# Kernel optimization log

Hardware: AMD Instinct MI355X
Metric: run time of the kernel (lower is better)

## Reference

```python
import jax, jax.numpy as jnp
import numpy as np

B, T, N, F = 4, 12, 4096, 32
NG = 14  # 14 gate GNNs: fx,fh,ix,ih,cx,ch,ox,oh,i,im,g,gm,o,om


def setup_inputs() -> dict:
    key = jax.random.key(0)
    k1, k2, k3 = jax.random.split(key, 3)
    x = jax.random.normal(k1, (B, T, N, F), dtype=jnp.float32)
    # weighted adjacency, scaled like row-normalized so adj@x stays O(1)
    adj = jax.random.uniform(k2, (B, N, N), dtype=jnp.float32) / N
    W = jax.random.normal(k3, (NG, F, 2 * F), dtype=jnp.float32) * (1.0 / np.sqrt(F))
    b = jnp.zeros((NG, 2 * F), dtype=jnp.float32)
    return {"x": x, "adj": adj, "W": W, "b": b}


def _wgc(v, adj, Wi, bi):
    # WeightedGraphConv: adj-matmul -> Dense(2F) -> GLU
    y = jnp.matmul(adj, v)                 # [B,N,F]
    z = jnp.matmul(y, Wi) + bi             # [B,N,2F]
    ls, rs = jnp.split(z, 2, axis=-1)
    return ls * jax.nn.sigmoid(rs)         # [B,N,F]


def reference(x, adj, W, b):
    Bb, Tt, Nn, Ff = x.shape
    ones = jnp.ones((Bb, Nn, Ff), dtype=x.dtype)
    h0, c0, m0 = ones, ones, ones

    def step(carry, xt):
        h, c, m = carry
        g = lambda i, v: _wgc(v, adj, W[i], b[i])
        f = jax.nn.sigmoid(g(0, xt) + g(1, h))     # forget
        i = jax.nn.sigmoid(g(2, xt) + g(3, h))     # input
        o = jax.nn.sigmoid(g(6, xt) + g(7, h))     # output
        c_new = f * c + i * jnp.tanh(g(4, xt) + g(5, h))
        h_mid = o * jnp.tanh(c_new)
        # memory-state gates (has_memory_state=True)
        i2 = jax.nn.sigmoid(g(8, h_mid) + g(9, m))
        gg = jax.nn.sigmoid(g(10, h_mid) + g(11, m))
        o2 = jax.nn.sigmoid(g(12, h_mid) + g(13, m))
        m_new = i2 * m + (1.0 - i2) * gg
        h_new = m_new * o2
        return (h_new, c_new, m_new), h_new

    (last_h, last_c, last_m), hs = jax.lax.scan(step, (h0, c0, m0), jnp.swapaxes(x, 0, 1))
    hidden_states = jnp.swapaxes(hs, 0, 1)  # [B,T,N,F]
    return hidden_states, last_h, last_c, last_m
```

## Files before the change

### kernel.cpp

```cpp
#include <hip/hip_runtime.h>


typedef __bf16 bf16_t;
typedef __bf16 bf16x8 __attribute__((ext_vector_type(8)));
typedef float  f32x4  __attribute__((ext_vector_type(4)));

#define DI __device__ __forceinline__

#define BB 4
#define TT 12
#define NN 4096
#define FF 32

DI float sigm(float x)  { return __builtin_amdgcn_rcpf(1.f + __expf(-x)); }
DI float tanh_f(float x){ float e = __expf(2.f * x); return 1.f - 2.f * __builtin_amdgcn_rcpf(e + 1.f); }

__global__ __launch_bounds__(256) void conv_adj_k(const float* __restrict__ a,
                                                  bf16_t* __restrict__ o) {
    size_t i = ((size_t)blockIdx.x * 256 + threadIdx.x) * 8;
    float4 v0 = *(const float4*)(a + i);
    float4 v1 = *(const float4*)(a + i + 4);
    union { uint4 u; bf16_t h[8]; } t;
    t.h[0] = (bf16_t)v0.x; t.h[1] = (bf16_t)v0.y; t.h[2] = (bf16_t)v0.z; t.h[3] = (bf16_t)v0.w;
    t.h[4] = (bf16_t)v1.x; t.h[5] = (bf16_t)v1.y; t.h[6] = (bf16_t)v1.z; t.h[7] = (bf16_t)v1.w;
    *(uint4*)(o + i) = t.u;
}

__global__ __launch_bounds__(256) void xpose_k(const float* __restrict__ x,
                                               bf16_t* __restrict__ xT) {
    const int b = blockIdx.z, t = blockIdx.y, n0 = blockIdx.x * 64;
    const int tid = threadIdx.x;
    __shared__ float tile[64][33];
    const float* src = x + (((size_t)(b * TT + t)) * NN + n0) * FF;
#pragma unroll
    for (int rr = 0; rr < 2; ++rr) {
        int idx = rr * 256 + tid;
        int row = idx >> 3, seg = idx & 7;
        float4 v = *(const float4*)(src + row * FF + seg * 4);
        tile[row][seg * 4 + 0] = v.x; tile[row][seg * 4 + 1] = v.y;
        tile[row][seg * 4 + 2] = v.z; tile[row][seg * 4 + 3] = v.w;
    }
    __syncthreads();
    const int f = tid >> 3, seg = tid & 7;
    union { uint4 u; bf16_t h[8]; } o;
#pragma unroll
    for (int j = 0; j < 8; ++j) o.h[j] = (bf16_t)tile[seg * 8 + j][f];
    *(uint4*)&xT[((size_t)(b * 384 + t * FF + f)) * NN + n0 + seg * 8] = o.u;
}

__global__ __launch_bounds__(256) void make_wfrag_k(const float* __restrict__ W,
                                                    bf16_t* __restrict__ Wf) {
    const int g = blockIdx.x, tid = threadIdx.x;
    const int ct = tid >> 6, lane = tid & 63;
    const int k0 = (lane >> 4) * 8, col = ct * 16 + (lane & 15);
    union { uint4 u; bf16_t h[8]; } t;
#pragma unroll
    for (int j = 0; j < 8; ++j) t.h[j] = (bf16_t)W[(g * 32 + k0 + j) * 64 + col];
    *(uint4*)&Wf[((g * 4 + ct) * 64 + lane) * 8] = t.u;
}

__global__ __launch_bounds__(256) void init_k(bf16_t* h_bf, bf16_t* hm_bf,
                                              float* c, float* m,
                                              float* Y1, float* Y2) {
    const int idx = blockIdx.x * 256 + threadIdx.x;
    Y1[idx] = 0.f;
    Y2[idx] = 0.f;
    if (idx < 524288) {
        const int b = idx >> 17, r = idx & 131071;
        h_bf[idx] = (bf16_t)1.f;
        hm_bf[(size_t)b * 262144 + 131072 + r] = (bf16_t)1.f;
        c[idx] = 1.f;
        m[idx] = 1.f;
    }
}

template <bool ABF, int S, int BS0, int BS1>
__global__ __launch_bounds__(256, 4) void gemm_splitk(const void* __restrict__ Ap,
                                                      const bf16_t* __restrict__ p0,
                                                      const bf16_t* __restrict__ p1,
                                                      float* __restrict__ Y) {
    const int b = blockIdx.z;
    const int row0 = blockIdx.x * 64;
    const int slice = blockIdx.y;
    const int tid = threadIdx.x, wave = tid >> 6, lane = tid & 63;
    const int mrow = lane & 15, quad = lane >> 4;
    __shared__ __align__(16) bf16_t Vs[64 * 256];
    const f32x4 zero = {0.f, 0.f, 0.f, 0.f};
    f32x4 acc[4];
#pragma unroll
    for (int i = 0; i < 4; ++i) acc[i] = zero;
    const int row = row0 + wave * 16 + mrow;
    const size_t arow = ((size_t)b << 24) + (size_t)row * NN;

    for (int stg = 0; stg < 4; ++stg) {
        const int k0 = slice * 1024 + stg * 256;
        bf16x8 af[8];
        if constexpr (ABF) {
            const bf16_t* ab = (const bf16_t*)Ap + arow + k0 + quad * 8;
#pragma unroll
            for (int s = 0; s < 8; ++s) af[s] = *(const bf16x8*)(ab + s * 32);
        } else {
            const float* ab = (const float*)Ap + arow + k0 + quad * 8;
#pragma unroll
            for (int s = 0; s < 8; ++s) {
                float4 v0 = *(const float4*)(ab + s * 32);
                float4 v1 = *(const float4*)(ab + s * 32 + 4);
                af[s][0] = (bf16_t)v0.x; af[s][1] = (bf16_t)v0.y;
                af[s][2] = (bf16_t)v0.z; af[s][3] = (bf16_t)v0.w;
                af[s][4] = (bf16_t)v1.x; af[s][5] = (bf16_t)v1.y;
                af[s][6] = (bf16_t)v1.z; af[s][7] = (bf16_t)v1.w;
            }
        }
#pragma unroll
        for (int rr = 0; rr < 8; ++rr) {
            const int idx = rr * 256 + tid;
            const int c = idx >> 5, ch = idx & 31;
            const bf16_t* src = (S < 64 && c >= S)
                ? p1 + ((size_t)b * BS1 + (c - S)) * NN
                : p0 + ((size_t)b * BS0 + c) * NN;
            *(uint4*)&Vs[c * 256 + (ch ^ (c & 7)) * 8] =
                *(const uint4*)(src + k0 + ch * 8);
        }
        __syncthreads();
#pragma unroll
        for (int s = 0; s < 8; ++s) {
#pragma unroll
            for (int ct = 0; ct < 4; ++ct) {
                const int c = ct * 16 + mrow;
                bf16x8 bfr = *(const bf16x8*)&Vs[c * 256 + (((s * 4 + quad) ^ (c & 7)) * 8)];
                acc[ct] = __builtin_amdgcn_mfma_f32_16x16x32_bf16(af[s], bfr, acc[ct], 0, 0, 0);
            }
        }
        __syncthreads();
    }
#pragma unroll
    for (int ct = 0; ct < 4; ++ct) {
        const int col = ct * 16 + mrow;
#pragma unroll
        for (int r = 0; r < 4; ++r) {
            const int orow = row0 + wave * 16 + quad * 4 + r;
            unsafeAtomicAdd(&Y[((size_t)b * NN + orow) * 64 + col], acc[ct][r]);
        }
    }
}

__global__ __launch_bounds__(256) void gates1_k(float* __restrict__ Y1,
                                                const bf16_t* __restrict__ Wf,
                                                const float* __restrict__ bias,
                                                float* __restrict__ c,
                                                bf16_t* __restrict__ hm_bf) {
    const int b = blockIdx.y, n0 = blockIdx.x * 64;
    const int tid = threadIdx.x, wave = tid >> 6, lane = tid & 63;
    const int mrow = lane & 15, quad = lane >> 4;
    const int nw = n0 + wave * 16;
    const f32x4 zero = {0.f, 0.f, 0.f, 0.f};
    float* yr = Y1 + ((size_t)b * NN + nw + mrow) * 64;
    float4 h0 = *(float4*)(yr + quad * 8);
    float4 h1 = *(float4*)(yr + quad * 8 + 4);
    float4 x0 = *(float4*)(yr + 32 + quad * 8);
    float4 x1 = *(float4*)(yr + 32 + quad * 8 + 4);
    const float4 z4 = {0.f, 0.f, 0.f, 0.f};
    *(float4*)(yr + quad * 8) = z4;      *(float4*)(yr + quad * 8 + 4) = z4;
    *(float4*)(yr + 32 + quad * 8) = z4; *(float4*)(yr + 32 + quad * 8 + 4) = z4;
    bf16x8 ah, ax;
    ah[0] = (bf16_t)h0.x; ah[1] = (bf16_t)h0.y; ah[2] = (bf16_t)h0.z; ah[3] = (bf16_t)h0.w;
    ah[4] = (bf16_t)h1.x; ah[5] = (bf16_t)h1.y; ah[6] = (bf16_t)h1.z; ah[7] = (bf16_t)h1.w;
    ax[0] = (bf16_t)x0.x; ax[1] = (bf16_t)x0.y; ax[2] = (bf16_t)x0.z; ax[3] = (bf16_t)x0.w;
    ax[4] = (bf16_t)x1.x; ax[5] = (bf16_t)x1.y; ax[6] = (bf16_t)x1.z; ax[7] = (bf16_t)x1.w;
    float gate[4][2][4];
#pragma unroll
    for (int gi = 0; gi < 4; ++gi) {
        const int ge = 2 * gi, go = ge + 1;
        f32x4 ze[4], zo[4];
#pragma unroll
        for (int ct = 0; ct < 4; ++ct) {
            bf16x8 we = *(const bf16x8*)&Wf[((ge * 4 + ct) * 64 + lane) * 8];
            bf16x8 wo = *(const bf16x8*)&Wf[((go * 4 + ct) * 64 + lane) * 8];
            ze[ct] = __builtin_amdgcn_mfma_f32_16x16x32_bf16(ax, we, zero, 0, 0, 0);
            zo[ct] = __builtin_amdgcn_mfma_f32_16x16x32_bf16(ah, wo, zero, 0, 0, 0);
            const float be = bias[ge * 64 + ct * 16 + mrow];
            const float bo = bias[go * 64 + ct * 16 + mrow];
#pragma unroll
            for (int r = 0; r < 4; ++r) { ze[ct][r] += be; zo[ct][r] += bo; }
        }
#pragma unroll
        for (int p = 0; p < 2; ++p)
#pragma unroll
            for (int r = 0; r < 4; ++r) {
                float s = ze[p][r] * sigm(ze[p + 2][r]) + zo[p][r] * sigm(zo[p + 2][r]);
                gate[gi][p][r] = (gi == 2) ? tanh_f(s) : sigm(s);
            }
    }
    __shared__ bf16_t hmT[32][64];
#pragma unroll
    for (int p = 0; p < 2; ++p)
#pragma unroll
        for (int r = 0; r < 4; ++r) {
            const int row = nw + quad * 4 + r, col = p * 16 + mrow;
            const size_t ci = ((size_t)b * NN + row) * FF + col;
            float cn = gate[0][p][r] * c[ci] + gate[1][p][r] * gate[2][p][r];
            c[ci] = cn;
            hmT[col][wave * 16 + quad * 4 + r] = (bf16_t)(gate[3][p][r] * tanh_f(cn));
        }
    __syncthreads();
    {
        const int col = tid >> 3, seg = tid & 7;
        union { uint4 u; bf16_t h[8]; } o;
#pragma unroll
        for (int j = 0; j < 8; ++j) o.h[j] = hmT[col][seg * 8 + j];
        *(uint4*)&hm_bf[((size_t)b * 64 + col) * NN + n0 + seg * 8] = o.u;
    }
}

__global__ __launch_bounds__(256) void gates2_k(float* __restrict__ Y2,
                                                const bf16_t* __restrict__ Wf,
                                                const float* __restrict__ bias,
                                                float* __restrict__ m,
                                                bf16_t* __restrict__ hm_bf,
                                                bf16_t* __restrict__ h_bf,
                                                float* __restrict__ hs, int t) {
    const int b = blockIdx.y, n0 = blockIdx.x * 64;
    const int tid = threadIdx.x, wave = tid >> 6, lane = tid & 63;
    const int mrow = lane & 15, quad = lane >> 4;
    const int nw = n0 + wave * 16;
    const f32x4 zero = {0.f, 0.f, 0.f, 0.f};
    float* yr = Y2 + ((size_t)b * NN + nw + mrow) * 64;
    float4 h0 = *(float4*)(yr + quad * 8);
    float4 h1 = *(float4*)(yr + quad * 8 + 4);
    float4 m0 = *(float4*)(yr + 32 + quad * 8);
    float4 m1 = *(float4*)(yr + 32 + quad * 8 + 4);
    const float4 z4 = {0.f, 0.f, 0.f, 0.f};
    *(float4*)(yr + quad * 8) = z4;      *(float4*)(yr + quad * 8 + 4) = z4;
    *(float4*)(yr + 32 + quad * 8) = z4; *(float4*)(yr + 32 + quad * 8 + 4) = z4;
    bf16x8 axh, axm;
    axh[0] = (bf16_t)h0.x; axh[1] = (bf16_t)h0.y; axh[2] = (bf16_t)h0.z; axh[3] = (bf16_t)h0.w;
    axh[4] = (bf16_t)h1.x; axh[5] = (bf16_t)h1.y; axh[6] = (bf16_t)h1.z; axh[7] = (bf16_t)h1.w;
    axm[0] = (bf16_t)m0.x; axm[1] = (bf16_t)m0.y; axm[2] = (bf16_t)m0.z; axm[3] = (bf16_t)m0.w;
    axm[4] = (bf16_t)m1.x; axm[5] = (bf16_t)m1.y; axm[6] = (bf16_t)m1.z; axm[7] = (bf16_t)m1.w;
    float gate[3][2][4];
#pragma unroll
    for (int gi = 0; gi < 3; ++gi) {
        const int ge = 8 + 2 * gi, go = ge + 1;
        f32x4 ze[4], zo[4];
#pragma unroll
        for (int ct = 0; ct < 4; ++ct) {
            bf16x8 we = *(const bf16x8*)&Wf[((ge * 4 + ct) * 64 + lane) * 8];
            bf16x8 wo = *(const bf16x8*)&Wf[((go * 4 + ct) * 64 + lane) * 8];
            ze[ct] = __builtin_amdgcn_mfma_f32_16x16x32_bf16(axh, we, zero, 0, 0, 0);
            zo[ct] = __builtin_amdgcn_mfma_f32_16x16x32_bf16(axm, wo, zero, 0, 0, 0);
            const float be = bias[ge * 64 + ct * 16 + mrow];
            const float bo = bias[go * 64 + ct * 16 + mrow];
#pragma unroll
            for (int r = 0; r < 4; ++r) { ze[ct][r] += be; zo[ct][r] += bo; }
        }
#pragma unroll
        for (int p = 0; p < 2; ++p)
#pragma unroll
            for (int r = 0; r < 4; ++r) {
                float s = ze[p][r] * sigm(ze[p + 2][r]) + zo[p][r] * sigm(zo[p + 2][r]);
                gate[gi][p][r] = sigm(s);
            }
    }
    __shared__ bf16_t mT[32][64];
    __shared__ bf16_t hT[32][64];
#pragma unroll
    for (int p = 0; p < 2; ++p)
#pragma unroll
        for (int r = 0; r < 4; ++r) {
            const int row = nw + quad * 4 + r, col = p * 16 + mrow;
            const size_t ci = ((size_t)b * NN + row) * FF + col;
            const float i2 = gate[0][p][r], gg = gate[1][p][r], o2 = gate[2][p][r];
            float mn = i2 * m[ci] + (1.f - i2) * gg;
            m[ci] = mn;
            float hn = mn * o2;
            hs[(((size_t)b * TT + t) * NN + row) * FF + col] = hn;
            mT[col][wave * 16 + quad * 4 + r] = (bf16_t)mn;
            hT[col][wave * 16 + quad * 4 + r] = (bf16_t)hn;
        }
    __syncthreads();
    {
        const int col = tid >> 3, seg = tid & 7;
        union { uint4 u; bf16_t h[8]; } om, oh;
#pragma unroll
        for (int j = 0; j < 8; ++j) { om.h[j] = mT[col][seg * 8 + j]; oh.h[j] = hT[col][seg * 8 + j]; }
        *(uint4*)&hm_bf[((size_t)b * 64 + 32 + col) * NN + n0 + seg * 8] = om.u;
        *(uint4*)&h_bf[((size_t)b * FF + col) * NN + n0 + seg * 8] = oh.u;
    }
}

__global__ __launch_bounds__(256) void finalize_k(const float* __restrict__ hs,
                                                  const float* __restrict__ c,
                                                  const float* __restrict__ m,
                                                  float* __restrict__ tail) {
    const int idx = blockIdx.x * 256 + threadIdx.x;
    const int b = idx >> 17, r = idx & 131071;
    tail[idx] = hs[((size_t)b * TT + (TT - 1)) * 131072 + r];
    tail[524288 + idx] = c[idx];
    tail[1048576 + idx] = m[idx];
}

extern "C" void kernel_launch(void* const* d_in, const int* in_sizes, int n_in,
                              void* d_out, int out_size, void* d_ws, size_t ws_size,
                              hipStream_t stream) {
    const float* x    = (const float*)d_in[0];
    const float* adj  = (const float*)d_in[1];
    const float* W    = (const float*)d_in[2];
    const float* bias = (const float*)d_in[3];
    float* out = (float*)d_out;

    char* ws = (char*)d_ws;
    size_t off = 0;
    auto carve = [&](size_t bytes) -> void* {
        void* p = ws + off;
        off += (bytes + 255) & ~(size_t)255;
        return p;
    };
    bf16_t* xT    = (bf16_t*)carve((size_t)BB * 384 * NN * 2);
    float*  Y1    = (float*)carve((size_t)BB * NN * 64 * 4);
    float*  Y2    = (float*)carve((size_t)BB * NN * 64 * 4);
    bf16_t* h_bf  = (bf16_t*)carve((size_t)BB * FF * NN * 2);
    bf16_t* hm_bf = (bf16_t*)carve((size_t)BB * 64 * NN * 2);
    bf16_t* Wf    = (bf16_t*)carve((size_t)14 * 4 * 64 * 8 * 2);
    float*  cbuf  = (float*)carve((size_t)BB * NN * FF * 4);
    float*  mbuf  = (float*)carve((size_t)BB * NN * FF * 4);
    const size_t adj_bytes = (size_t)BB * NN * NN * 2;
    const bool abf = (ws_size >= off + adj_bytes);
    bf16_t* adj_bf = abf ? (bf16_t*)carve(adj_bytes) : nullptr;

    if (abf) conv_adj_k<<<32768, 256, 0, stream>>>(adj, adj_bf);
    make_wfrag_k<<<14, 256, 0, stream>>>(W, Wf);
    xpose_k<<<dim3(64, TT, BB), 256, 0, stream>>>(x, xT);
    init_k<<<4096, 256, 0, stream>>>(h_bf, hm_bf, cbuf, mbuf, Y1, Y2);

    const dim3 ggrid(64, 4, BB);
    for (int t = 0; t < TT; ++t) {
        const bf16_t* xts = xT + (size_t)t * 32 * NN;
        if (abf) gemm_splitk<true, 32, 32, 384><<<ggrid, 256, 0, stream>>>(adj_bf, h_bf, xts, Y1);
        else     gemm_splitk<false, 32, 32, 384><<<ggrid, 256, 0, stream>>>(adj, h_bf, xts, Y1);
        gates1_k<<<dim3(64, BB), 256, 0, stream>>>(Y1, Wf, bias, cbuf, hm_bf);
        if (abf) gemm_splitk<true, 64, 64, 64><<<ggrid, 256, 0, stream>>>(adj_bf, hm_bf, hm_bf, Y2);
        else     gemm_splitk<false, 64, 64, 64><<<ggrid, 256, 0, stream>>>(adj, hm_bf, hm_bf, Y2);
        gates2_k<<<dim3(64, BB), 256, 0, stream>>>(Y2, Wf, bias, mbuf, hm_bf, h_bf, out, t);
    }
    finalize_k<<<2048, 256, 0, stream>>>(out, cbuf, mbuf, out + (size_t)BB * TT * NN * FF);
}
```

Baseline: 1.412 ms.

## Fuse adjacency GEMM with gate epilogue and drop split-K atomics

```diff
diff --git a/kernel.cpp b/kernel.cpp
--- a/kernel.cpp
+++ b/kernel.cpp
@@ -59,232 +59,192 @@
     *(uint4*)&Wf[((g * 4 + ct) * 64 + lane) * 8] = t.u;
 }
 
-__global__ __launch_bounds__(256) void init_k(bf16_t* h_bf, bf16_t* hm_bf,
-                                              float* c, float* m,
-                                              float* Y1, float* Y2) {
+__global__ __launch_bounds__(256) void init_k(bf16_t* h_bf, bf16_t* m0,
+                                              float* c, float* m) {
     const int idx = blockIdx.x * 256 + threadIdx.x;
-    Y1[idx] = 0.f;
-    Y2[idx] = 0.f;
-    if (idx < 524288) {
-        const int b = idx >> 17, r = idx & 131071;
-        h_bf[idx] = (bf16_t)1.f;
-        hm_bf[(size_t)b * 262144 + 131072 + r] = (bf16_t)1.f;
-        c[idx] = 1.f;
-        m[idx] = 1.f;
-    }
-}
-
-template <bool ABF, int S, int BS0, int BS1>
-__global__ __launch_bounds__(256, 4) void gemm_splitk(const void* __restrict__ Ap,
-                                                      const bf16_t* __restrict__ p0,
-                                                      const bf16_t* __restrict__ p1,
-                                                      float* __restrict__ Y) {
-    const int b = blockIdx.z;
-    const int row0 = blockIdx.x * 64;
-    const int slice = blockIdx.y;
-    const int tid = threadIdx.x, wave = tid >> 6, lane = tid & 63;
+    h_bf[idx] = (bf16_t)1.f;
+    m0[idx]   = (bf16_t)1.f;
+    c[idx] = 1.f;
+    m[idx] = 1.f;
+}
+
+template <bool ABF, bool G1>
+__global__ __launch_bounds__(512, 2) void gg_k(
+    const void* __restrict__ Ap,
+    const bf16_t* __restrict__ p0, const bf16_t* __restrict__ p1,
+    const bf16_t* __restrict__ Wf, const float* __restrict__ bias,
+    float* __restrict__ cm, bf16_t* __restrict__ hmW,
+    bf16_t* __restrict__ hb, float* __restrict__ hs, int t)
+{
+    constexpr int BS0 = 32;
+    constexpr int BS1 = G1 ? 384 : 32;
+    const int b = blockIdx.y, n0 = blockIdx.x * 64;
+    const int tid = threadIdx.x;
+    const int wave = tid >> 6, lane = tid & 63;
     const int mrow = lane & 15, quad = lane >> 4;
-    __shared__ __align__(16) bf16_t Vs[64 * 256];
-    const f32x4 zero = {0.f, 0.f, 0.f, 0.f};
+    const int wr = wave & 3, kh = wave >> 2;
+    const int gtid = tid & 255;
+    const int cw = gtid >> 5, ch = gtid & 31;
+
+    __shared__ __align__(16) bf16_t Vs[2][64 * 256];
+    __shared__ float Yl[2][64][68];
+    __shared__ bf16_t t0T[32][64];
+    __shared__ bf16_t t1T[32][64];
+
+    const int row = n0 + wr * 16 + mrow;
+    const size_t arow = ((size_t)b << 24) + (size_t)row * NN;
+    const f32x4 zero4 = {0.f, 0.f, 0.f, 0.f};
     f32x4 acc[4];
-#pragma unroll
-    for (int i = 0; i < 4; ++i) acc[i] = zero;
-    const int row = row0 + wave * 16 + mrow;
-    const size_t arow = ((size_t)b << 24) + (size_t)row * NN;
-
-    for (int stg = 0; stg < 4; ++stg) {
-        const int k0 = slice * 1024 + stg * 256;
-        bf16x8 af[8];
+    acc[0] = zero4; acc[1] = zero4; acc[2] = zero4; acc[3] = zero4;
+
+    const bf16_t* srow[8];
+    int loff[8];
+#pragma unroll
+    for (int rr = 0; rr < 8; ++rr) {
+        const int c = rr * 8 + cw;
+        const bf16_t* base = (c >= 32) ? p1 + ((size_t)b * BS1 + (c - 32)) * NN
+                                       : p0 + ((size_t)b * BS0 + c) * NN;
+        srow[rr] = base + kh * 2048 + ch * 8;
+        loff[rr] = c * 256 + ((ch ^ (c & 7)) * 8);
+    }
+    const bf16_t* Abase  = (const bf16_t*)Ap + arow + kh * 2048 + quad * 8;
+    const float*  AbaseF = (const float*)Ap + arow + kh * 2048 + quad * 8;
+
+    uint4  brg[8];
+    bf16x8 af[2][8];
+#pragma unroll
+    for (int rr = 0; rr < 8; ++rr) brg[rr] = *(const uint4*)(srow[rr]);
+    if constexpr (ABF) {
+#pragma unroll
+        for (int s = 0; s < 8; ++s) af[0][s] = *(const bf16x8*)(Abase + s * 32);
+    }
+#pragma unroll
+    for (int rr = 0; rr < 8; ++rr) *(uint4*)&Vs[kh][loff[rr]] = brg[rr];
+    __syncthreads();
+
+#pragma unroll
+    for (int stg = 0; stg < 8; ++stg) {
+        const int cur = stg & 1, nxt = cur ^ 1;
+        if (stg < 7) {
+#pragma unroll
+            for (int rr = 0; rr < 8; ++rr)
+                brg[rr] = *(const uint4*)(srow[rr] + (stg + 1) * 256);
+            if constexpr (ABF) {
+#pragma unroll
+                for (int s = 0; s < 8; ++s)
+                    af[nxt][s] = *(const bf16x8*)(Abase + (stg + 1) * 256 + s * 32);
+            }
+        }
+        bf16x8 afs[8];
         if constexpr (ABF) {
-            const bf16_t* ab = (const bf16_t*)Ap + arow + k0 + quad * 8;
-#pragma unroll
-            for (int s = 0; s < 8; ++s) af[s] = *(const bf16x8*)(ab + s * 32);
+#pragma unroll
+            for (int s = 0; s < 8; ++s) afs[s] = af[cur][s];
         } else {
-            const float* ab = (const float*)Ap + arow + k0 + quad * 8;
 #pragma unroll
             for (int s = 0; s < 8; ++s) {
-                float4 v0 = *(const float4*)(ab + s * 32);
-                float4 v1 = *(const float4*)(ab + s * 32 + 4);
-                af[s][0] = (bf16_t)v0.x; af[s][1] = (bf16_t)v0.y;
-                af[s][2] = (bf16_t)v0.z; af[s][3] = (bf16_t)v0.w;
-                af[s][4] = (bf16_t)v1.x; af[s][5] = (bf16_t)v1.y;
-                af[s][6] = (bf16_t)v1.z; af[s][7] = (bf16_t)v1.w;
-            }
-        }
-#pragma unroll
-        for (int rr = 0; rr < 8; ++rr) {
-            const int idx = rr * 256 + tid;
-            const int c = idx >> 5, ch = idx & 31;
-            const bf16_t* src = (S < 64 && c >= S)
-                ? p1 + ((size_t)b * BS1 + (c - S)) * NN
-                : p0 + ((size_t)b * BS0 + c) * NN;
-            *(uint4*)&Vs[c * 256 + (ch ^ (c & 7)) * 8] =
-                *(const uint4*)(src + k0 + ch * 8);
-        }
-        __syncthreads();
+                float4 v0 = *(const float4*)(AbaseF + stg * 256 + s * 32);
+                float4 v1 = *(const float4*)(AbaseF + stg * 256 + s * 32 + 4);
+                afs[s][0] = (bf16_t)v0.x; afs[s][1] = (bf16_t)v0.y;
+                afs[s][2] = (bf16_t)v0.z; afs[s][3] = (bf16_t)v0.w;
+                afs[s][4] = (bf16_t)v1.x; afs[s][5] = (bf16_t)v1.y;
+                afs[s][6] = (bf16_t)v1.z; afs[s][7] = (bf16_t)v1.w;
+            }
+        }
 #pragma unroll
         for (int s = 0; s < 8; ++s) {
 #pragma unroll
             for (int ct = 0; ct < 4; ++ct) {
                 const int c = ct * 16 + mrow;
-                bf16x8 bfr = *(const bf16x8*)&Vs[c * 256 + (((s * 4 + quad) ^ (c & 7)) * 8)];
-                acc[ct] = __builtin_amdgcn_mfma_f32_16x16x32_bf16(af[s], bfr, acc[ct], 0, 0, 0);
+                bf16x8 bfr = *(const bf16x8*)&Vs[kh][c * 256 + (((s * 4 + quad) ^ (c & 7)) * 8)];
+                acc[ct] = __builtin_amdgcn_mfma_f32_16x16x32_bf16(afs[s], bfr, acc[ct], 0, 0, 0);
             }
         }
         __syncthreads();
-    }
-#pragma unroll
-    for (int ct = 0; ct < 4; ++ct) {
-        const int col = ct * 16 + mrow;
-#pragma unroll
-        for (int r = 0; r < 4; ++r) {
-            const int orow = row0 + wave * 16 + quad * 4 + r;
-            unsafeAtomicAdd(&Y[((size_t)b * NN + orow) * 64 + col], acc[ct][r]);
-        }
-    }
-}
-
-__global__ __launch_bounds__(256) void gates1_k(float* __restrict__ Y1,
-                                                const bf16_t* __restrict__ Wf,
-                                                const float* __restrict__ bias,
-                                                float* __restrict__ c,
-                                                bf16_t* __restrict__ hm_bf) {
-    const int b = blockIdx.y, n0 = blockIdx.x * 64;
-    const int tid = threadIdx.x, wave = tid >> 6, lane = tid & 63;
-    const int mrow = lane & 15, quad = lane >> 4;
-    const int nw = n0 + wave * 16;
-    const f32x4 zero = {0.f, 0.f, 0.f, 0.f};
-    float* yr = Y1 + ((size_t)b * NN + nw + mrow) * 64;
-    float4 h0 = *(float4*)(yr + quad * 8);
-    float4 h1 = *(float4*)(yr + quad * 8 + 4);
-    float4 x0 = *(float4*)(yr + 32 + quad * 8);
-    float4 x1 = *(float4*)(yr + 32 + quad * 8 + 4);
-    const float4 z4 = {0.f, 0.f, 0.f, 0.f};
-    *(float4*)(yr + quad * 8) = z4;      *(float4*)(yr + quad * 8 + 4) = z4;
-    *(float4*)(yr + 32 + quad * 8) = z4; *(float4*)(yr + 32 + quad * 8 + 4) = z4;
-    bf16x8 ah, ax;
-    ah[0] = (bf16_t)h0.x; ah[1] = (bf16_t)h0.y; ah[2] = (bf16_t)h0.z; ah[3] = (bf16_t)h0.w;
-    ah[4] = (bf16_t)h1.x; ah[5] = (bf16_t)h1.y; ah[6] = (bf16_t)h1.z; ah[7] = (bf16_t)h1.w;
-    ax[0] = (bf16_t)x0.x; ax[1] = (bf16_t)x0.y; ax[2] = (bf16_t)x0.z; ax[3] = (bf16_t)x0.w;
-    ax[4] = (bf16_t)x1.x; ax[5] = (bf16_t)x1.y; ax[6] = (bf16_t)x1.z; ax[7] = (bf16_t)x1.w;
-    float gate[4][2][4];
-#pragma unroll
-    for (int gi = 0; gi < 4; ++gi) {
-        const int ge = 2 * gi, go = ge + 1;
-        f32x4 ze[4], zo[4];
-#pragma unroll
-        for (int ct = 0; ct < 4; ++ct) {
-            bf16x8 we = *(const bf16x8*)&Wf[((ge * 4 + ct) * 64 + lane) * 8];
-            bf16x8 wo = *(const bf16x8*)&Wf[((go * 4 + ct) * 64 + lane) * 8];
-            ze[ct] = __builtin_amdgcn_mfma_f32_16x16x32_bf16(ax, we, zero, 0, 0, 0);
-            zo[ct] = __builtin_amdgcn_mfma_f32_16x16x32_bf16(ah, wo, zero, 0, 0, 0);
-            const float be = bias[ge * 64 + ct * 16 + mrow];
-            const float bo = bias[go * 64 + ct * 16 + mrow];
-#pragma unroll
-            for (int r = 0; r < 4; ++r) { ze[ct][r] += be; zo[ct][r] += bo; }
+        if (stg < 7) {
+#pragma unroll
+            for (int rr = 0; rr < 8; ++rr) *(uint4*)&Vs[kh][loff[rr]] = brg[rr];
+            __syncthreads();
+        }
+    }
+
+#pragma unroll
+    for (int ct = 0; ct < 4; ++ct)
+#pragma unroll
+        for (int r = 0; r < 4; ++r)
+            Yl[kh][wr * 16 + quad * 4 + r][ct * 16 + mrow] = acc[ct][r];
+    __syncthreads();
+
+    if (wave < 4) {
+        const int rl = wave * 16 + mrow;
+        const float* ya = &Yl[0][rl][0];
+        const float* yb = &Yl[1][rl][0];
+        bf16x8 f0, f1;
+#pragma unroll
+        for (int j = 0; j < 8; ++j) {
+            f0[j] = (bf16_t)(ya[quad * 8 + j] + yb[quad * 8 + j]);
+            f1[j] = (bf16_t)(ya[32 + quad * 8 + j] + yb[32 + quad * 8 + j]);
+        }
+        constexpr int NGI = G1 ? 4 : 3;
+        constexpr int GB  = G1 ? 0 : 8;
+        float gate[NGI][2][4];
+#pragma unroll
+        for (int gi = 0; gi < NGI; ++gi) {
+            const int ge = GB + 2 * gi, go = ge + 1;
+            f32x4 ze[4], zo[4];
+#pragma unroll
+            for (int ct = 0; ct < 4; ++ct) {
+                bf16x8 we = *(const bf16x8*)&Wf[((ge * 4 + ct) * 64 + lane) * 8];
+                bf16x8 wo = *(const bf16x8*)&Wf[((go * 4 + ct) * 64 + lane) * 8];
+                ze[ct] = __builtin_amdgcn_mfma_f32_16x16x32_bf16(G1 ? f1 : f0, we, zero4, 0, 0, 0);
+                zo[ct] = __builtin_amdgcn_mfma_f32_16x16x32_bf16(G1 ? f0 : f1, wo, zero4, 0, 0, 0);
+                const float be = bias[ge * 64 + ct * 16 + mrow];
+                const float bo = bias[go * 64 + ct * 16 + mrow];
+#pragma unroll
+                for (int r = 0; r < 4; ++r) { ze[ct][r] += be; zo[ct][r] += bo; }
+            }
+#pragma unroll
+            for (int p = 0; p < 2; ++p)
+#pragma unroll
+                for (int r = 0; r < 4; ++r) {
+                    float s = ze[p][r] * sigm(ze[p + 2][r]) + zo[p][r] * sigm(zo[p + 2][r]);
+                    gate[gi][p][r] = (G1 && gi == 2) ? tanh_f(s) : sigm(s);
+                }
         }
 #pragma unroll
         for (int p = 0; p < 2; ++p)
 #pragma unroll
             for (int r = 0; r < 4; ++r) {
-                float s = ze[p][r] * sigm(ze[p + 2][r]) + zo[p][r] * sigm(zo[p + 2][r]);
-                gate[gi][p][r] = (gi == 2) ? tanh_f(s) : sigm(s);
-            }
-    }
-    __shared__ bf16_t hmT[32][64];
-#pragma unroll
-    for (int p = 0; p < 2; ++p)
-#pragma unroll
-        for (int r = 0; r < 4; ++r) {
-            const int row = nw + quad * 4 + r, col = p * 16 + mrow;
-            const size_t ci = ((size_t)b * NN + row) * FF + col;
-            float cn = gate[0][p][r] * c[ci] + gate[1][p][r] * gate[2][p][r];
-            c[ci] = cn;
-            hmT[col][wave * 16 + quad * 4 + r] = (bf16_t)(gate[3][p][r] * tanh_f(cn));
-        }
+                const int rloc = wave * 16 + quad * 4 + r;
+                const int rowg = n0 + rloc, col = p * 16 + mrow;
+                const size_t ci = ((size_t)b * NN + rowg) * FF + col;
+                if constexpr (G1) {
+                    float cn = gate[0][p][r] * cm[ci] + gate[1][p][r] * gate[2][p][r];
+                    cm[ci] = cn;
+                    t0T[col][rloc] = (bf16_t)(gate[3][p][r] * tanh_f(cn));
+                } else {
+                    const float i2 = gate[0][p][r], gg = gate[1][p][r], o2 = gate[2][p][r];
+                    float mn = i2 * cm[ci] + (1.f - i2) * gg;
+                    cm[ci] = mn;
+                    float hn = mn * o2;
+                    hs[(((size_t)b * TT + t) * NN + rowg) * FF + col] = hn;
+                    t0T[col][rloc] = (bf16_t)mn;
+                    t1T[col][rloc] = (bf16_t)hn;
+                }
+            }
+    }
     __syncthreads();
-    {
+    if (tid < 256) {
         const int col = tid >> 3, seg = tid & 7;
-        union { uint4 u; bf16_t h[8]; } o;
-#pragma unroll
-        for (int j = 0; j < 8; ++j) o.h[j] = hmT[col][seg * 8 + j];
-        *(uint4*)&hm_bf[((size_t)b * 64 + col) * NN + n0 + seg * 8] = o.u;
-    }
-}
-
-__global__ __launch_bounds__(256) void gates2_k(float* __restrict__ Y2,
-                                                const bf16_t* __restrict__ Wf,
-                                                const float* __restrict__ bias,
-                                                float* __restrict__ m,
-                                                bf16_t* __restrict__ hm_bf,
-                                                bf16_t* __restrict__ h_bf,
-                                                float* __restrict__ hs, int t) {
-    const int b = blockIdx.y, n0 = blockIdx.x * 64;
-    const int tid = threadIdx.x, wave = tid >> 6, lane = tid & 63;
-    const int mrow = lane & 15, quad = lane >> 4;
-    const int nw = n0 + wave * 16;
-    const f32x4 zero = {0.f, 0.f, 0.f, 0.f};
-    float* yr = Y2 + ((size_t)b * NN + nw + mrow) * 64;
-    float4 h0 = *(float4*)(yr + quad * 8);
-    float4 h1 = *(float4*)(yr + quad * 8 + 4);
-    float4 m0 = *(float4*)(yr + 32 + quad * 8);
-    float4 m1 = *(float4*)(yr + 32 + quad * 8 + 4);
-    const float4 z4 = {0.f, 0.f, 0.f, 0.f};
-    *(float4*)(yr + quad * 8) = z4;      *(float4*)(yr + quad * 8 + 4) = z4;
-    *(float4*)(yr + 32 + quad * 8) = z4; *(float4*)(yr + 32 + quad * 8 + 4) = z4;
-    bf16x8 axh, axm;
-    axh[0] = (bf16_t)h0.x; axh[1] = (bf16_t)h0.y; axh[2] = (bf16_t)h0.z; axh[3] = (bf16_t)h0.w;
-    axh[4] = (bf16_t)h1.x; axh[5] = (bf16_t)h1.y; axh[6] = (bf16_t)h1.z; axh[7] = (bf16_t)h1.w;
-    axm[0] = (bf16_t)m0.x; axm[1] = (bf16_t)m0.y; axm[2] = (bf16_t)m0.z; axm[3] = (bf16_t)m0.w;
-    axm[4] = (bf16_t)m1.x; axm[5] = (bf16_t)m1.y; axm[6] = (bf16_t)m1.z; axm[7] = (bf16_t)m1.w;
-    float gate[3][2][4];
-#pragma unroll
-    for (int gi = 0; gi < 3; ++gi) {
-        const int ge = 8 + 2 * gi, go = ge + 1;
-        f32x4 ze[4], zo[4];
-#pragma unroll
-        for (int ct = 0; ct < 4; ++ct) {
-            bf16x8 we = *(const bf16x8*)&Wf[((ge * 4 + ct) * 64 + lane) * 8];
-            bf16x8 wo = *(const bf16x8*)&Wf[((go * 4 + ct) * 64 + lane) * 8];
-            ze[ct] = __builtin_amdgcn_mfma_f32_16x16x32_bf16(axh, we, zero, 0, 0, 0);
-            zo[ct] = __builtin_amdgcn_mfma_f32_16x16x32_bf16(axm, wo, zero, 0, 0, 0);
-            const float be = bias[ge * 64 + ct * 16 + mrow];
-            const float bo = bias[go * 64 + ct * 16 + mrow];
-#pragma unroll
-            for (int r = 0; r < 4; ++r) { ze[ct][r] += be; zo[ct][r] += bo; }
-        }
-#pragma unroll
-        for (int p = 0; p < 2; ++p)
-#pragma unroll
-            for (int r = 0; r < 4; ++r) {
-                float s = ze[p][r] * sigm(ze[p + 2][r]) + zo[p][r] * sigm(zo[p + 2][r]);
-                gate[gi][p][r] = sigm(s);
-            }
-    }
-    __shared__ bf16_t mT[32][64];
-    __shared__ bf16_t hT[32][64];
-#pragma unroll
-    for (int p = 0; p < 2; ++p)
-#pragma unroll
-        for (int r = 0; r < 4; ++r) {
-            const int row = nw + quad * 4 + r, col = p * 16 + mrow;
-            const size_t ci = ((size_t)b * NN + row) * FF + col;
-            const float i2 = gate[0][p][r], gg = gate[1][p][r], o2 = gate[2][p][r];
-            float mn = i2 * m[ci] + (1.f - i2) * gg;
-            m[ci] = mn;
-            float hn = mn * o2;
-            hs[(((size_t)b * TT + t) * NN + row) * FF + col] = hn;
-            mT[col][wave * 16 + quad * 4 + r] = (bf16_t)mn;
-            hT[col][wave * 16 + quad * 4 + r] = (bf16_t)hn;
-        }
-    __syncthreads();
-    {
-        const int col = tid >> 3, seg = tid & 7;
-        union { uint4 u; bf16_t h[8]; } om, oh;
-#pragma unroll
-        for (int j = 0; j < 8; ++j) { om.h[j] = mT[col][seg * 8 + j]; oh.h[j] = hT[col][seg * 8 + j]; }
-        *(uint4*)&hm_bf[((size_t)b * 64 + 32 + col) * NN + n0 + seg * 8] = om.u;
-        *(uint4*)&h_bf[((size_t)b * FF + col) * NN + n0 + seg * 8] = oh.u;
+        union { uint4 u; bf16_t h[8]; } o0;
+#pragma unroll
+        for (int j = 0; j < 8; ++j) o0.h[j] = t0T[col][seg * 8 + j];
+        *(uint4*)&hmW[((size_t)b * 32 + col) * NN + n0 + seg * 8] = o0.u;
+        if constexpr (!G1) {
+            union { uint4 u; bf16_t h[8]; } o1;
+#pragma unroll
+            for (int j = 0; j < 8; ++j) o1.h[j] = t1T[col][seg * 8 + j];
+            *(uint4*)&hb[((size_t)b * FF + col) * NN + n0 + seg * 8] = o1.u;
+        }
     }
 }
 
@@ -316,10 +276,10 @@
         return p;
     };
     bf16_t* xT    = (bf16_t*)carve((size_t)BB * 384 * NN * 2);
-    float*  Y1    = (float*)carve((size_t)BB * NN * 64 * 4);
-    float*  Y2    = (float*)carve((size_t)BB * NN * 64 * 4);
-    bf16_t* h_bf  = (bf16_t*)carve((size_t)BB * FF * NN * 2);
-    bf16_t* hm_bf = (bf16_t*)carve((size_t)BB * 64 * NN * 2);
+    bf16_t* h_bf  = (bf16_t*)carve((size_t)BB * 32 * NN * 2);
+    bf16_t* hmid  = (bf16_t*)carve((size_t)BB * 32 * NN * 2);
+    bf16_t* mbf0  = (bf16_t*)carve((size_t)BB * 32 * NN * 2);
+    bf16_t* mbf1  = (bf16_t*)carve((size_t)BB * 32 * NN * 2);
     bf16_t* Wf    = (bf16_t*)carve((size_t)14 * 4 * 64 * 8 * 2);
     float*  cbuf  = (float*)carve((size_t)BB * NN * FF * 4);
     float*  mbuf  = (float*)carve((size_t)BB * NN * FF * 4);
@@ -330,17 +290,24 @@
     if (abf) conv_adj_k<<<32768, 256, 0, stream>>>(adj, adj_bf);
     make_wfrag_k<<<14, 256, 0, stream>>>(W, Wf);
     xpose_k<<<dim3(64, TT, BB), 256, 0, stream>>>(x, xT);
-    init_k<<<4096, 256, 0, stream>>>(h_bf, hm_bf, cbuf, mbuf, Y1, Y2);
-
-    const dim3 ggrid(64, 4, BB);
+    init_k<<<2048, 256, 0, stream>>>(h_bf, mbf0, cbuf, mbuf);
+
+    const dim3 grid(64, BB);
     for (int t = 0; t < TT; ++t) {
         const bf16_t* xts = xT + (size_t)t * 32 * NN;
-        if (abf) gemm_splitk<true, 32, 32, 384><<<ggrid, 256, 0, stream>>>(adj_bf, h_bf, xts, Y1);
-        else     gemm_splitk<false, 32, 32, 384><<<ggrid, 256, 0, stream>>>(adj, h_bf, xts, Y1);
-        gates1_k<<<dim3(64, BB), 256, 0, stream>>>(Y1, Wf, bias, cbuf, hm_bf);
-        if (abf) gemm_splitk<true, 64, 64, 64><<<ggrid, 256, 0, stream>>>(adj_bf, hm_bf, hm_bf, Y2);
-        else     gemm_splitk<false, 64, 64, 64><<<ggrid, 256, 0, stream>>>(adj, hm_bf, hm_bf, Y2);
-        gates2_k<<<dim3(64, BB), 256, 0, stream>>>(Y2, Wf, bias, mbuf, hm_bf, h_bf, out, t);
+        bf16_t* mrd = (t & 1) ? mbf1 : mbf0;
+        bf16_t* mwr = (t & 1) ? mbf0 : mbf1;
+        if (abf) {
+            gg_k<true,  true ><<<grid, 512, 0, stream>>>(adj_bf, h_bf, xts, Wf, bias,
+                                                         cbuf, hmid, nullptr, nullptr, 0);
+            gg_k<true,  false><<<grid, 512, 0, stream>>>(adj_bf, hmid, mrd, Wf, bias,
+                                                         mbuf, mwr, h_bf, out, t);
+        } else {
+            gg_k<false, true ><<<grid, 512, 0, stream>>>(adj, h_bf, xts, Wf, bias,
+                                                         cbuf, hmid, nullptr, nullptr, 0);
+            gg_k<false, false><<<grid, 512, 0, stream>>>(adj, hmid, mrd, Wf, bias,
+                                                         mbuf, mwr, h_bf, out, t);
+        }
     }
     finalize_k<<<2048, 256, 0, stream>>>(out, cbuf, mbuf, out + (size_t)BB * TT * NN * FF);
 }
```

Result: slower. 1.944 ms (+37.7%).
